# Optimization experiments

Hardware: AMD Instinct MI355X
Metric: run time of the kernel (lower is better)

The kernel has to match this reference:

```python
import jax, jax.numpy as jnp
import numpy as np

N = 100_000
E = 3_200_000
FEAT, HID, EMB = 128, 32, 16
NEG_SLOPE = 0.2


def setup_inputs() -> dict:
    key = jax.random.key(0)
    ks = jax.random.split(key, 12)
    x = jax.random.normal(ks[0], (N, FEAT), dtype=jnp.float32)
    ei = jax.random.randint(ks[1], (2, E), 0, N, dtype=jnp.int32)
    ew = jax.random.uniform(ks[2], (E, 1), dtype=jnp.float32)
    # GATConv layer 1: feat_dim -> hidden_dim, heads=1
    s1 = 1.0 / np.sqrt(FEAT)
    W1 = jax.random.normal(ks[3], (FEAT, HID), dtype=jnp.float32) * s1
    a_src1 = jax.random.normal(ks[4], (HID,), dtype=jnp.float32) * (1.0 / np.sqrt(HID))
    a_dst1 = jax.random.normal(ks[5], (HID,), dtype=jnp.float32) * (1.0 / np.sqrt(HID))
    b1 = jnp.zeros((HID,), dtype=jnp.float32)
    # GATConv layer 2: hidden_dim -> embed_dim, heads=1
    s2 = 1.0 / np.sqrt(HID)
    W2 = jax.random.normal(ks[6], (HID, EMB), dtype=jnp.float32) * s2
    a_src2 = jax.random.normal(ks[7], (EMB,), dtype=jnp.float32) * (1.0 / np.sqrt(EMB))
    a_dst2 = jax.random.normal(ks[8], (EMB,), dtype=jnp.float32) * (1.0 / np.sqrt(EMB))
    b2 = jnp.zeros((EMB,), dtype=jnp.float32)
    return {"x": x, "ei": ei, "ew": ew, "W1": W1, "a_src1": a_src1,
            "a_dst1": a_dst1, "b1": b1, "W2": W2, "a_src2": a_src2,
            "a_dst2": a_dst2, "b2": b2}


def gat_conv(x, src, dst, W, a_src, a_dst, b):
    """PyG GATConv, heads=1, add_self_loops=True, edge_attr ignored (edge_dim=None)."""
    n = x.shape[0]
    h = x @ W                              # [N, C]
    al_s = h @ a_src                       # [N]
    al_d = h @ a_dst                       # [N]
    loop = jnp.arange(n, dtype=src.dtype)
    srcs = jnp.concatenate([src, loop])    # [E+N]
    dsts = jnp.concatenate([dst, loop])
    alpha = jax.nn.leaky_relu(al_s[srcs] + al_d[dsts], NEG_SLOPE)
    # segment softmax over edges grouped by destination node
    m = jax.ops.segment_max(alpha, dsts, num_segments=n)
    e = jnp.exp(alpha - m[dsts])
    denom = jax.ops.segment_sum(e, dsts, num_segments=n)
    coef = e / (denom[dsts] + 1e-16)
    out = jax.ops.segment_sum(coef[:, None] * h[srcs], dsts, num_segments=n)
    return out + b


def reference(x, ei, ew, W1, a_src1, a_dst1, b1, W2, a_src2, a_dst2, b2):
    # eval mode: DropEdge and Dropout are identity; ew unused by GATConv (edge_dim=None)
    src, dst = ei[0], ei[1]
    h = gat_conv(x, src, dst, W1, a_src1, a_dst1, b1)
    h = jax.nn.relu(h)
    return gat_conv(h, src, dst, W2, a_src2, a_dst2, b2)
```

## Files before the change

kernel.cpp:

```cpp
#include <hip/hip_runtime.h>
#include <hip/hip_fp16.h>

#define FEAT 128
#define HID 32
#define EMB 16
#define NEG 0.2f

#define BSH 8
#define BIN_NODES 256
#define NBMAX 400
#define CH 8192
#define SRCBITS 17
#define SRCMASK 0x1FFFF

struct __align__(8)  H4 { __half2 a, b; };
struct __align__(16) H8 { __half2 a, b, c, d; };

__device__ __forceinline__ float lrelu(float a) { return a > 0.0f ? a : NEG * a; }

__global__ __launch_bounds__(256) void k_zero_int(int* p, int n) {
    int i = (int)(blockIdx.x * 256 + threadIdx.x);
    if (i < n) p[i] = 0;
}

__global__ __launch_bounds__(256) void k_bincnt(const int* __restrict__ ei, int E_,
                                                int Nn, int* __restrict__ binCnt) {
    __shared__ int h[NBMAX];
    int nb = (Nn + BIN_NODES - 1) >> BSH;
    for (int i = threadIdx.x; i < nb; i += 256) h[i] = 0;
    __syncthreads();
    int stride = (int)(gridDim.x * 256);
    for (int i = (int)(blockIdx.x * 256 + threadIdx.x); i < E_; i += stride)
        atomicAdd(&h[ei[(size_t)E_ + i] >> BSH], 1);
    __syncthreads();
    for (int i = threadIdx.x; i < nb; i += 256)
        if (h[i]) atomicAdd(&binCnt[i], h[i]);
}

__global__ __launch_bounds__(512) void k_binscan(const int* __restrict__ binCnt,
                                                 int* __restrict__ binstart,
                                                 int* __restrict__ bin_pos,
                                                 int* __restrict__ rowptr,
                                                 int Nn, int E_) {
    __shared__ int s[512];
    int nb = (Nn + BIN_NODES - 1) >> BSH;
    int t = (int)threadIdx.x;
    s[t] = (t < nb) ? binCnt[t] : 0;
    __syncthreads();
    for (int off = 1; off < 512; off <<= 1) {
        int v = (t >= off) ? s[t - off] : 0;
        __syncthreads();
        s[t] += v;
        __syncthreads();
    }
    if (t <= nb) binstart[t] = (t == 0) ? 0 : s[t - 1];
    if (t < nb) bin_pos[t] = (t == 0) ? 0 : s[t - 1];
    if (t == 0) rowptr[Nn] = E_;
}

__global__ __launch_bounds__(1024) void k_part(const int* __restrict__ ei, int E_,
                                               int Nn, int* __restrict__ bin_pos,
                                               int* __restrict__ packed) {
    __shared__ int hist[NBMAX];
    __shared__ int lofs[NBMAX];
    __shared__ int pos[NBMAX];
    __shared__ int gbase[NBMAX];
    __shared__ int sscan[512];
    __shared__ int staged[CH];
    __shared__ unsigned short sbin[CH];
    int nb = (Nn + BIN_NODES - 1) >> BSH;
    int base = (int)(blockIdx.x * CH);
    int nE = min(CH, E_ - base);
    int t = (int)threadIdx.x;
    for (int i = t; i < nb; i += 1024) hist[i] = 0;
    __syncthreads();

    int myw[CH / 1024];
    int myb[CH / 1024];
#pragma unroll
    for (int k = 0; k < CH / 1024; ++k) {
        int i = t + k * 1024;
        int w = 0, b_ = -1;
        if (i < nE) {
            int s_ = ei[base + i];
            int d_ = ei[(size_t)E_ + base + i];
            b_ = d_ >> BSH;
            w = ((d_ & (BIN_NODES - 1)) << SRCBITS) | s_;
            atomicAdd(&hist[b_], 1);
        }
        myw[k] = w;
        myb[k] = b_;
    }
    __syncthreads();
    if (t < 512) sscan[t] = (t < nb) ? hist[t] : 0;
    __syncthreads();
    for (int off = 1; off < 512; off <<= 1) {
        int v = 0;
        if (t < 512 && t >= off) v = sscan[t - off];
        __syncthreads();
        if (t < 512) sscan[t] += v;
        __syncthreads();
    }
    for (int i = t; i < nb; i += 1024) {
        int ex = (i == 0) ? 0 : sscan[i - 1];
        lofs[i] = ex;
        pos[i] = ex;
    }
    __syncthreads();
#pragma unroll
    for (int k = 0; k < CH / 1024; ++k) {
        if (myb[k] >= 0) {
            int p = atomicAdd(&pos[myb[k]], 1);
            staged[p] = myw[k];
            sbin[p] = (unsigned short)myb[k];
        }
    }
    __syncthreads();
    for (int i = t; i < nb; i += 1024)
        gbase[i] = hist[i] ? atomicAdd(&bin_pos[i], hist[i]) : 0;
    __syncthreads();
    for (int i = t; i < nE; i += 1024) {
        int b_ = sbin[i];
        packed[gbase[b_] + (i - lofs[b_])] = staged[i];
    }
}

__global__ __launch_bounds__(1024) void k_build(const int* __restrict__ binstart,
                                                int Nn,
                                                const int* __restrict__ packed,
                                                int* __restrict__ csr,
                                                int* __restrict__ rowptr) {
    __shared__ int ncnt[BIN_NODES];
    __shared__ int npos[BIN_NODES];
    __shared__ int sscan[BIN_NODES];
    int b = (int)blockIdx.x;
    int s = binstart[b], e = binstart[b + 1];
    int cnt = e - s;
    int nb0 = b << BSH;
    int nodes = min(BIN_NODES, Nn - nb0);
    int t = (int)threadIdx.x;
    if (t < BIN_NODES) ncnt[t] = 0;
    __syncthreads();
    for (int i = t; i < cnt; i += 1024)
        atomicAdd(&ncnt[(packed[s + i] >> SRCBITS) & 255], 1);
    __syncthreads();
    if (t < BIN_NODES) sscan[t] = ncnt[t];
    __syncthreads();
    for (int off = 1; off < BIN_NODES; off <<= 1) {
        int v = 0;
        if (t < BIN_NODES && t >= off) v = sscan[t - off];
        __syncthreads();
        if (t < BIN_NODES) sscan[t] += v;
        __syncthreads();
    }
    if (t < BIN_NODES) {
        int ex = (t == 0) ? 0 : sscan[t - 1];
        npos[t] = ex;
        if (t < nodes) rowptr[nb0 + t] = s + ex;
    }
    __syncthreads();
    for (int i = t; i < cnt; i += 1024) {
        int w = packed[s + i];
        int p = atomicAdd(&npos[(w >> SRCBITS) & 255], 1);
        csr[s + p] = w & SRCMASK;
    }
}

__global__ __launch_bounds__(256) void k_h1(
    const float* __restrict__ x, const float* __restrict__ W1,
    const float* __restrict__ a_s, const float* __restrict__ a_d,
    __half* __restrict__ h1h, float* __restrict__ als, float* __restrict__ ald,
    int Nn)
{
    int row = (int)(blockIdx.x * 256 + threadIdx.x);
    if (row >= Nn) return;
    const float4* xr = (const float4*)(x + (size_t)row * FEAT);
    float acc[HID];
#pragma unroll
    for (int c = 0; c < HID; ++c) acc[c] = 0.0f;
#pragma unroll 4
    for (int k4 = 0; k4 < FEAT / 4; ++k4) {
        float4 xv = xr[k4];
        const float* Wr = W1 + k4 * 4 * HID;
#pragma unroll
        for (int c = 0; c < HID; ++c)
            acc[c] += xv.x * Wr[c] + xv.y * Wr[HID + c]
                    + xv.z * Wr[2 * HID + c] + xv.w * Wr[3 * HID + c];
    }
    float ps = 0.0f, pd = 0.0f;
#pragma unroll
    for (int c = 0; c < HID; ++c) {
        ps += acc[c] * a_s[c];
        pd += acc[c] * a_d[c];
    }
    H8* dst = (H8*)(h1h + (size_t)row * HID);
#pragma unroll
    for (int q = 0; q < 4; ++q) {
        H8 v;
        v.a = __float22half2_rn(make_float2(acc[8 * q + 0], acc[8 * q + 1]));
        v.b = __float22half2_rn(make_float2(acc[8 * q + 2], acc[8 * q + 3]));
        v.c = __float22half2_rn(make_float2(acc[8 * q + 4], acc[8 * q + 5]));
        v.d = __float22half2_rn(make_float2(acc[8 * q + 6], acc[8 * q + 7]));
        dst[q] = v;
    }
    als[row] = ps;
    ald[row] = pd;
}

__global__ __launch_bounds__(256) void k_agg1(
    const int* __restrict__ rowptr, const int* __restrict__ csr,
    const __half* __restrict__ h1h, const float* __restrict__ als,
    const float* __restrict__ ald, const float* __restrict__ b1,
    const float* __restrict__ W2, const float* __restrict__ a_s2,
    const float* __restrict__ a_d2,
    __half* __restrict__ h2h, float* __restrict__ als2, float* __restrict__ ald2,
    int Nn)
{
    int n = (int)(blockIdx.x * 32 + (threadIdx.x >> 3));
    if (n >= Nn) return;
    int l = threadIdx.x & 7;
    const H4* hp = (const H4*)h1h + l;
    float aldn = ald[n];
    float wself = __expf(lrelu(als[n] + aldn));
    H4 rs = hp[(size_t)n * 8];
    float2 pa = __half22float2(rs.a);
    float2 pb = __half22float2(rs.b);
    float s0x = wself * pa.x, s0y = wself * pa.y;
    float s0z = wself * pb.x, s0w = wself * pb.y;
    float s1x = 0, s1y = 0, s1z = 0, s1w = 0;
    float s2x = 0, s2y = 0, s2z = 0, s2w = 0;
    float s3x = 0, s3y = 0, s3z = 0, s3w = 0;
    float den = wself;
    int e = rowptr[n], e1 = rowptr[n + 1];
    for (; e + 8 <= e1; e += 8) {
        int i0 = csr[e + 0];
        int i1 = csr[e + 1];
        int i2 = csr[e + 2];
        int i3 = csr[e + 3];
        int i4 = csr[e + 4];
        int i5 = csr[e + 5];
        int i6 = csr[e + 6];
        int i7 = csr[e + 7];
        H4 g0 = hp[(size_t)i0 * 8];
        H4 g1 = hp[(size_t)i1 * 8];
        H4 g2 = hp[(size_t)i2 * 8];
        H4 g3 = hp[(size_t)i3 * 8];
        H4 g4 = hp[(size_t)i4 * 8];
        H4 g5 = hp[(size_t)i5 * 8];
        H4 g6 = hp[(size_t)i6 * 8];
        H4 g7 = hp[(size_t)i7 * 8];
        float a0 = als[i0], a1 = als[i1], a2 = als[i2], a3 = als[i3];
        float a4 = als[i4], a5 = als[i5], a6 = als[i6], a7 = als[i7];
        float w0 = __expf(lrelu(a0 + aldn));
        float w1 = __expf(lrelu(a1 + aldn));
        float w2 = __expf(lrelu(a2 + aldn));
        float w3 = __expf(lrelu(a3 + aldn));
        float w4 = __expf(lrelu(a4 + aldn));
        float w5 = __expf(lrelu(a5 + aldn));
        float w6 = __expf(lrelu(a6 + aldn));
        float w7 = __expf(lrelu(a7 + aldn));
        float2 f0a = __half22float2(g0.a), f0b = __half22float2(g0.b);
        float2 f1a = __half22float2(g1.a), f1b = __half22float2(g1.b);
        float2 f2a = __half22float2(g2.a), f2b = __half22float2(g2.b);
        float2 f3a = __half22float2(g3.a), f3b = __half22float2(g3.b);
        float2 f4a = __half22float2(g4.a), f4b = __half22float2(g4.b);
        float2 f5a = __half22float2(g5.a), f5b = __half22float2(g5.b);
        float2 f6a = __half22float2(g6.a), f6b = __half22float2(g6.b);
        float2 f7a = __half22float2(g7.a), f7b = __half22float2(g7.b);
        s0x += w0 * f0a.x + w4 * f4a.x; s0y += w0 * f0a.y + w4 * f4a.y;
        s0z += w0 * f0b.x + w4 * f4b.x; s0w += w0 * f0b.y + w4 * f4b.y;
        s1x += w1 * f1a.x + w5 * f5a.x; s1y += w1 * f1a.y + w5 * f5a.y;
        s1z += w1 * f1b.x + w5 * f5b.x; s1w += w1 * f1b.y + w5 * f5b.y;
        s2x += w2 * f2a.x + w6 * f6a.x; s2y += w2 * f2a.y + w6 * f6a.y;
        s2z += w2 * f2b.x + w6 * f6b.x; s2w += w2 * f2b.y + w6 * f6b.y;
        s3x += w3 * f3a.x + w7 * f7a.x; s3y += w3 * f3a.y + w7 * f7a.y;
        s3z += w3 * f3b.x + w7 * f7b.x; s3w += w3 * f3b.y + w7 * f7b.y;
        den += ((w0 + w1) + (w2 + w3)) + ((w4 + w5) + (w6 + w7));
    }
    for (; e + 4 <= e1; e += 4) {
        int i0 = csr[e + 0];
        int i1 = csr[e + 1];
        int i2 = csr[e + 2];
        int i3 = csr[e + 3];
        H4 g0 = hp[(size_t)i0 * 8];
        H4 g1 = hp[(size_t)i1 * 8];
        H4 g2 = hp[(size_t)i2 * 8];
        H4 g3 = hp[(size_t)i3 * 8];
        float a0 = als[i0], a1 = als[i1], a2 = als[i2], a3 = als[i3];
        float w0 = __expf(lrelu(a0 + aldn));
        float w1 = __expf(lrelu(a1 + aldn));
        float w2 = __expf(lrelu(a2 + aldn));
        float w3 = __expf(lrelu(a3 + aldn));
        float2 f0a = __half22float2(g0.a), f0b = __half22float2(g0.b);
        float2 f1a = __half22float2(g1.a), f1b = __half22float2(g1.b);
        float2 f2a = __half22float2(g2.a), f2b = __half22float2(g2.b);
        float2 f3a = __half22float2(g3.a), f3b = __half22float2(g3.b);
        s0x += w0 * f0a.x; s0y += w0 * f0a.y; s0z += w0 * f0b.x; s0w += w0 * f0b.y;
        s1x += w1 * f1a.x; s1y += w1 * f1a.y; s1z += w1 * f1b.x; s1w += w1 * f1b.y;
        s2x += w2 * f2a.x; s2y += w2 * f2a.y; s2z += w2 * f2b.x; s2w += w2 * f2b.y;
        s3x += w3 * f3a.x; s3y += w3 * f3a.y; s3z += w3 * f3b.x; s3w += w3 * f3b.y;
        den += (w0 + w1) + (w2 + w3);
    }
    for (; e < e1; ++e) {
        int s = csr[e];
        float we = __expf(lrelu(als[s] + aldn));
        H4 g = hp[(size_t)s * 8];
        float2 fa = __half22float2(g.a), fb = __half22float2(g.b);
        s0x += we * fa.x; s0y += we * fa.y; s0z += we * fb.x; s0w += we * fb.y;
        den += we;
    }
    float inv = 1.0f / den;
    float gx = fmaxf((s0x + s1x + s2x + s3x) * inv + b1[4 * l + 0], 0.0f);
    float gy = fmaxf((s0y + s1y + s2y + s3y) * inv + b1[4 * l + 1], 0.0f);
    float gz = fmaxf((s0z + s1z + s2z + s3z) * inv + b1[4 * l + 2], 0.0f);
    float gw = fmaxf((s0w + s1w + s2w + s3w) * inv + b1[4 * l + 3], 0.0f);
    float hc0 = 0.0f, hc1 = 0.0f;
#pragma unroll
    for (int tt = 0; tt < 8; ++tt) {
        float bx = __shfl(gx, tt, 8);
        float by = __shfl(gy, tt, 8);
        float bz = __shfl(gz, tt, 8);
        float bw = __shfl(gw, tt, 8);
        const float* wp = &W2[(4 * tt) * EMB];
        hc0 += bx * wp[l] + by * wp[EMB + l]
             + bz * wp[2 * EMB + l] + bw * wp[3 * EMB + l];
        hc1 += bx * wp[l + 8] + by * wp[EMB + l + 8]
             + bz * wp[2 * EMB + l + 8] + bw * wp[3 * EMB + l + 8];
    }
    h2h[(size_t)n * EMB + l]     = __float2half(hc0);
    h2h[(size_t)n * EMB + l + 8] = __float2half(hc1);
    float ps = hc0 * a_s2[l] + hc1 * a_s2[l + 8];
    float pd = hc0 * a_d2[l] + hc1 * a_d2[l + 8];
    for (int m = 1; m < 8; m <<= 1) {
        ps += __shfl_xor(ps, m, 8);
        pd += __shfl_xor(pd, m, 8);
    }
    if (l == 0) { als2[n] = ps; ald2[n] = pd; }
}

__global__ __launch_bounds__(256) void k_agg2(
    const int* __restrict__ rowptr, const int* __restrict__ csr,
    const __half* __restrict__ h2h, const float* __restrict__ als,
    const float* __restrict__ ald, const float* __restrict__ b2,
    float* __restrict__ out, int Nn)
{
    int n = (int)(blockIdx.x * 32 + (threadIdx.x >> 3));
    if (n >= Nn) return;
    int l = threadIdx.x & 7;
    const __half2* hp = (const __half2*)h2h + l;
    float aldn = ald[n];
    float wself = __expf(lrelu(als[n] + aldn));
    float2 sv = __half22float2(hp[(size_t)n * 8]);
    float s0x = wself * sv.x, s0y = wself * sv.y;
    float s1x = 0, s1y = 0, s2x = 0, s2y = 0, s3x = 0, s3y = 0;
    float den = wself;
    int e = rowptr[n], e1 = rowptr[n + 1];
    for (; e + 8 <= e1; e += 8) {
        int i0 = csr[e + 0];
        int i1 = csr[e + 1];
        int i2 = csr[e + 2];
        int i3 = csr[e + 3];
        int i4 = csr[e + 4];
        int i5 = csr[e + 5];
        int i6 = csr[e + 6];
        int i7 = csr[e + 7];
        __half2 g0 = hp[(size_t)i0 * 8];
        __half2 g1 = hp[(size_t)i1 * 8];
        __half2 g2 = hp[(size_t)i2 * 8];
        __half2 g3 = hp[(size_t)i3 * 8];
        __half2 g4 = hp[(size_t)i4 * 8];
        __half2 g5 = hp[(size_t)i5 * 8];
        __half2 g6 = hp[(size_t)i6 * 8];
        __half2 g7 = hp[(size_t)i7 * 8];
        float a0 = als[i0], a1 = als[i1], a2 = als[i2], a3 = als[i3];
        float a4 = als[i4], a5 = als[i5], a6 = als[i6], a7 = als[i7];
        float w0 = __expf(lrelu(a0 + aldn));
        float w1 = __expf(lrelu(a1 + aldn));
        float w2 = __expf(lrelu(a2 + aldn));
        float w3 = __expf(lrelu(a3 + aldn));
        float w4 = __expf(lrelu(a4 + aldn));
        float w5 = __expf(lrelu(a5 + aldn));
        float w6 = __expf(lrelu(a6 + aldn));
        float w7 = __expf(lrelu(a7 + aldn));
        float2 f0 = __half22float2(g0), f1 = __half22float2(g1);
        float2 f2 = __half22float2(g2), f3 = __half22float2(g3);
        float2 f4 = __half22float2(g4), f5 = __half22float2(g5);
        float2 f6 = __half22float2(g6), f7 = __half22float2(g7);
        s0x += w0 * f0.x + w4 * f4.x; s0y += w0 * f0.y + w4 * f4.y;
        s1x += w1 * f1.x + w5 * f5.x; s1y += w1 * f1.y + w5 * f5.y;
        s2x += w2 * f2.x + w6 * f6.x; s2y += w2 * f2.y + w6 * f6.y;
        s3x += w3 * f3.x + w7 * f7.x; s3y += w3 * f3.y + w7 * f7.y;
        den += ((w0 + w1) + (w2 + w3)) + ((w4 + w5) + (w6 + w7));
    }
    for (; e + 4 <= e1; e += 4) {
        int i0 = csr[e + 0];
        int i1 = csr[e + 1];
        int i2 = csr[e + 2];
        int i3 = csr[e + 3];
        __half2 g0 = hp[(size_t)i0 * 8];
        __half2 g1 = hp[(size_t)i1 * 8];
        __half2 g2 = hp[(size_t)i2 * 8];
        __half2 g3 = hp[(size_t)i3 * 8];
        float a0 = als[i0], a1 = als[i1], a2 = als[i2], a3 = als[i3];
        float w0 = __expf(lrelu(a0 + aldn));
        float w1 = __expf(lrelu(a1 + aldn));
        float w2 = __expf(lrelu(a2 + aldn));
        float w3 = __expf(lrelu(a3 + aldn));
        float2 f0 = __half22float2(g0), f1 = __half22float2(g1);
        float2 f2 = __half22float2(g2), f3 = __half22float2(g3);
        s0x += w0 * f0.x; s0y += w0 * f0.y;
        s1x += w1 * f1.x; s1y += w1 * f1.y;
        s2x += w2 * f2.x; s2y += w2 * f2.y;
        s3x += w3 * f3.x; s3y += w3 * f3.y;
        den += (w0 + w1) + (w2 + w3);
    }
    for (; e < e1; ++e) {
        int s = csr[e];
        float we = __expf(lrelu(als[s] + aldn));
        float2 f = __half22float2(hp[(size_t)s * 8]);
        s0x += we * f.x; s0y += we * f.y;
        den += we;
    }
    float inv = 1.0f / den;
    float2 r;
    r.x = (s0x + s1x + s2x + s3x) * inv + b2[2 * l];
    r.y = (s0y + s1y + s2y + s3y) * inv + b2[2 * l + 1];
    *(float2*)(out + (size_t)n * EMB + 2 * l) = r;
}

extern "C" void kernel_launch(void* const* d_in, const int* in_sizes, int n_in,
                              void* d_out, int out_size, void* d_ws, size_t ws_size,
                              hipStream_t stream)
{
    const float* x   = (const float*)d_in[0];
    const int*   ei  = (const int*)d_in[1];
    const float* W1  = (const float*)d_in[3];
    const float* as1 = (const float*)d_in[4];
    const float* ad1 = (const float*)d_in[5];
    const float* b1  = (const float*)d_in[6];
    const float* W2  = (const float*)d_in[7];
    const float* as2 = (const float*)d_in[8];
    const float* ad2 = (const float*)d_in[9];
    const float* b2  = (const float*)d_in[10];
    float* out = (float*)d_out;

    const int Nn = in_sizes[0] / FEAT;
    const int E_ = in_sizes[1] / 2;
    const int nb = (Nn + BIN_NODES - 1) >> BSH;

    __half* h1h   = (__half*)d_ws;
    float* als1   = (float*)(h1h + (size_t)Nn * HID);
    float* ald1   = als1 + Nn;
    __half* h2h   = (__half*)(ald1 + Nn);
    float* als2p  = (float*)(h2h + (size_t)Nn * EMB);
    float* ald2p  = als2p + Nn;
    int* rowptr   = (int*)(ald2p + Nn);
    int* binCnt   = rowptr + Nn + 1;
    int* binstart = binCnt + NBMAX;
    int* bin_pos  = binstart + NBMAX + 1;
    int* packedr  = bin_pos + NBMAX;
    int* packed   = (int*)(((uintptr_t)packedr + 15) & ~(uintptr_t)15);
    int* csr      = packed + E_;

    k_zero_int<<<(nb + 255) / 256, 256, 0, stream>>>(binCnt, nb);
    k_bincnt<<<1024, 256, 0, stream>>>(ei, E_, Nn, binCnt);
    k_binscan<<<1, 512, 0, stream>>>(binCnt, binstart, bin_pos, rowptr, Nn, E_);
    k_part<<<(E_ + CH - 1) / CH, 1024, 0, stream>>>(ei, E_, Nn, bin_pos, packed);
    k_build<<<nb, 1024, 0, stream>>>(binstart, Nn, packed, csr, rowptr);

    k_h1<<<(Nn + 255) / 256, 256, 0, stream>>>(x, W1, as1, ad1, h1h, als1, ald1, Nn);
    k_agg1<<<(Nn + 31) / 32, 256, 0, stream>>>(rowptr, csr, h1h, als1, ald1,
                                               b1, W2, as2, ad2,
                                               h2h, als2p, ald2p, Nn);
    k_agg2<<<(Nn + 31) / 32, 256, 0, stream>>>(rowptr, csr, h2h, als2p, ald2p,
                                               b2, out, Nn);
}
```

Before: 310.6 us.

## Fuse layer-1 projection, bin counting and bin scan into one kernel

Replaces the zeroing kernel, the bin-count kernel, the single-block bin scan and the separate layer-1 projection kernel with one 1024-block kernel plus a memset. Each block projects its rows through W1 and also counts destination bins. The last block to finish, found with an atomic ticket counter, does the exclusive scan over the bin counts. This is meant to cut kernel launches and inter-kernel gaps and to let the compute-heavy projection overlap the atomic-heavy counting. In exchange it adds a threadfence and ticket dependency, and it relies on the fixed grid covering every node row.

```diff
diff --git a/kernel.cpp b/kernel.cpp
--- a/kernel.cpp
+++ b/kernel.cpp
@@ -12,50 +12,97 @@
 #define CH 8192
 #define SRCBITS 17
 #define SRCMASK 0x1FFFF
+#define PREGRID 1024
 
 struct __align__(8)  H4 { __half2 a, b; };
 struct __align__(16) H8 { __half2 a, b, c, d; };
 
 __device__ __forceinline__ float lrelu(float a) { return a > 0.0f ? a : NEG * a; }
 
-__global__ __launch_bounds__(256) void k_zero_int(int* p, int n) {
-    int i = (int)(blockIdx.x * 256 + threadIdx.x);
-    if (i < n) p[i] = 0;
-}
-
-__global__ __launch_bounds__(256) void k_bincnt(const int* __restrict__ ei, int E_,
-                                                int Nn, int* __restrict__ binCnt) {
+__global__ __launch_bounds__(256) void k_pre(
+    const int* __restrict__ ei, int E_, int Nn,
+    const float* __restrict__ x, const float* __restrict__ W1,
+    const float* __restrict__ a_s, const float* __restrict__ a_d,
+    __half* __restrict__ h1h, float* __restrict__ als, float* __restrict__ ald,
+    int* __restrict__ binCnt, int* __restrict__ done,
+    int* __restrict__ binstart, int* __restrict__ bin_pos,
+    int* __restrict__ rowptr)
+{
     __shared__ int h[NBMAX];
+    __shared__ int vals[512];
+    __shared__ int ps[256];
+    __shared__ int ticket_s;
     int nb = (Nn + BIN_NODES - 1) >> BSH;
-    for (int i = threadIdx.x; i < nb; i += 256) h[i] = 0;
-    __syncthreads();
+    int tid = (int)threadIdx.x;
+    for (int i = tid; i < nb; i += 256) h[i] = 0;
+    __syncthreads();
+
+    int row = (int)(blockIdx.x * 256 + tid);
+    if (row < Nn) {
+        const float4* xr = (const float4*)(x + (size_t)row * FEAT);
+        float acc[HID];
+#pragma unroll
+        for (int c = 0; c < HID; ++c) acc[c] = 0.0f;
+#pragma unroll 4
+        for (int k4 = 0; k4 < FEAT / 4; ++k4) {
+            float4 xv = xr[k4];
+            const float* Wr = W1 + k4 * 4 * HID;
+#pragma unroll
+            for (int c = 0; c < HID; ++c)
+                acc[c] += xv.x * Wr[c] + xv.y * Wr[HID + c]
+                        + xv.z * Wr[2 * HID + c] + xv.w * Wr[3 * HID + c];
+        }
+        float psum = 0.0f, pdum = 0.0f;
+#pragma unroll
+        for (int c = 0; c < HID; ++c) {
+            psum += acc[c] * a_s[c];
+            pdum += acc[c] * a_d[c];
+        }
+        H8* dst = (H8*)(h1h + (size_t)row * HID);
+#pragma unroll
+        for (int q = 0; q < 4; ++q) {
+            H8 v;
+            v.a = __float22half2_rn(make_float2(acc[8 * q + 0], acc[8 * q + 1]));
+            v.b = __float22half2_rn(make_float2(acc[8 * q + 2], acc[8 * q + 3]));
+            v.c = __float22half2_rn(make_float2(acc[8 * q + 4], acc[8 * q + 5]));
+            v.d = __float22half2_rn(make_float2(acc[8 * q + 6], acc[8 * q + 7]));
+            dst[q] = v;
+        }
+        als[row] = psum;
+        ald[row] = pdum;
+    }
+
     int stride = (int)(gridDim.x * 256);
-    for (int i = (int)(blockIdx.x * 256 + threadIdx.x); i < E_; i += stride)
+    for (int i = (int)(blockIdx.x * 256 + tid); i < E_; i += stride)
         atomicAdd(&h[ei[(size_t)E_ + i] >> BSH], 1);
     __syncthreads();
-    for (int i = threadIdx.x; i < nb; i += 256)
+    for (int i = tid; i < nb; i += 256)
         if (h[i]) atomicAdd(&binCnt[i], h[i]);
-}
-
-__global__ __launch_bounds__(512) void k_binscan(const int* __restrict__ binCnt,
-                                                 int* __restrict__ binstart,
-                                                 int* __restrict__ bin_pos,
-                                                 int* __restrict__ rowptr,
-                                                 int Nn, int E_) {
-    __shared__ int s[512];
-    int nb = (Nn + BIN_NODES - 1) >> BSH;
-    int t = (int)threadIdx.x;
-    s[t] = (t < nb) ? binCnt[t] : 0;
-    __syncthreads();
-    for (int off = 1; off < 512; off <<= 1) {
-        int v = (t >= off) ? s[t - off] : 0;
-        __syncthreads();
-        s[t] += v;
-        __syncthreads();
-    }
-    if (t <= nb) binstart[t] = (t == 0) ? 0 : s[t - 1];
-    if (t < nb) bin_pos[t] = (t == 0) ? 0 : s[t - 1];
-    if (t == 0) rowptr[Nn] = E_;
+
+    __syncthreads();
+    __threadfence();
+    if (tid == 0) ticket_s = atomicAdd(done, 1);
+    __syncthreads();
+    if (ticket_s != (int)gridDim.x - 1) return;
+
+    for (int i = tid; i < nb; i += 256) vals[i] = atomicAdd(&binCnt[i], 0);
+    for (int i = nb + tid; i < 512; i += 256) vals[i] = 0;
+    __syncthreads();
+    int a = vals[2 * tid], b = vals[2 * tid + 1];
+    int csum = a + b;
+    ps[tid] = csum;
+    __syncthreads();
+    for (int off = 1; off < 256; off <<= 1) {
+        int v = (tid >= off) ? ps[tid - off] : 0;
+        __syncthreads();
+        ps[tid] += v;
+        __syncthreads();
+    }
+    int excl = ps[tid] - csum;
+    if (2 * tid < nb)     { binstart[2 * tid] = excl;         bin_pos[2 * tid] = excl; }
+    if (2 * tid + 1 < nb) { binstart[2 * tid + 1] = excl + a; bin_pos[2 * tid + 1] = excl + a; }
+    if (tid == 255) binstart[nb] = ps[255];
+    if (tid == 0) rowptr[Nn] = E_;
 }
 
 __global__ __launch_bounds__(1024) void k_part(const int* __restrict__ ei, int E_,
@@ -164,47 +211,6 @@
         int p = atomicAdd(&npos[(w >> SRCBITS) & 255], 1);
         csr[s + p] = w & SRCMASK;
     }
-}
-
-__global__ __launch_bounds__(256) void k_h1(
-    const float* __restrict__ x, const float* __restrict__ W1,
-    const float* __restrict__ a_s, const float* __restrict__ a_d,
-    __half* __restrict__ h1h, float* __restrict__ als, float* __restrict__ ald,
-    int Nn)
-{
-    int row = (int)(blockIdx.x * 256 + threadIdx.x);
-    if (row >= Nn) return;
-    const float4* xr = (const float4*)(x + (size_t)row * FEAT);
-    float acc[HID];
-#pragma unroll
-    for (int c = 0; c < HID; ++c) acc[c] = 0.0f;
-#pragma unroll 4
-    for (int k4 = 0; k4 < FEAT / 4; ++k4) {
-        float4 xv = xr[k4];
-        const float* Wr = W1 + k4 * 4 * HID;
-#pragma unroll
-        for (int c = 0; c < HID; ++c)
-            acc[c] += xv.x * Wr[c] + xv.y * Wr[HID + c]
-                    + xv.z * Wr[2 * HID + c] + xv.w * Wr[3 * HID + c];
-    }
-    float ps = 0.0f, pd = 0.0f;
-#pragma unroll
-    for (int c = 0; c < HID; ++c) {
-        ps += acc[c] * a_s[c];
-        pd += acc[c] * a_d[c];
-    }
-    H8* dst = (H8*)(h1h + (size_t)row * HID);
-#pragma unroll
-    for (int q = 0; q < 4; ++q) {
-        H8 v;
-        v.a = __float22half2_rn(make_float2(acc[8 * q + 0], acc[8 * q + 1]));
-        v.b = __float22half2_rn(make_float2(acc[8 * q + 2], acc[8 * q + 3]));
-        v.c = __float22half2_rn(make_float2(acc[8 * q + 4], acc[8 * q + 5]));
-        v.d = __float22half2_rn(make_float2(acc[8 * q + 6], acc[8 * q + 7]));
-        dst[q] = v;
-    }
-    als[row] = ps;
-    ald[row] = pd;
 }
 
 __global__ __launch_bounds__(256) void k_agg1(
@@ -456,19 +462,21 @@
     float* ald2p  = als2p + Nn;
     int* rowptr   = (int*)(ald2p + Nn);
     int* binCnt   = rowptr + Nn + 1;
-    int* binstart = binCnt + NBMAX;
+    int* done     = binCnt + NBMAX;
+    int* binstart = done + 1;
     int* bin_pos  = binstart + NBMAX + 1;
     int* packedr  = bin_pos + NBMAX;
     int* packed   = (int*)(((uintptr_t)packedr + 15) & ~(uintptr_t)15);
     int* csr      = packed + E_;
 
-    k_zero_int<<<(nb + 255) / 256, 256, 0, stream>>>(binCnt, nb);
-    k_bincnt<<<1024, 256, 0, stream>>>(ei, E_, Nn, binCnt);
-    k_binscan<<<1, 512, 0, stream>>>(binCnt, binstart, bin_pos, rowptr, Nn, E_);
+    hipMemsetAsync(binCnt, 0, (NBMAX + 1) * sizeof(int), stream);
+
+    k_pre<<<PREGRID, 256, 0, stream>>>(ei, E_, Nn, x, W1, as1, ad1,
+                                       h1h, als1, ald1,
+                                       binCnt, done, binstart, bin_pos, rowptr);
     k_part<<<(E_ + CH - 1) / CH, 1024, 0, stream>>>(ei, E_, Nn, bin_pos, packed);
     k_build<<<nb, 1024, 0, stream>>>(binstart, Nn, packed, csr, rowptr);
 
-    k_h1<<<(Nn + 255) / 256, 256, 0, stream>>>(x, W1, as1, ad1, h1h, als1, ald1, Nn);
     k_agg1<<<(Nn + 31) / 32, 256, 0, stream>>>(rowptr, csr, h1h, als1, ald1,
                                                b1, W2, as2, ad2,
                                                h2h, als2p, ald2p, Nn);
```

Result: slower. 400.6 us (+29.0%).
